# Kernel optimization log

Measured on AMD Instinct MI355X. Metric: run time of the kernel, lower is better.

The kernel has to match this reference:

```python
import jax, jax.numpy as jnp
import numpy as np
from jax import lax

GAMMA = 2.0
BLANK = 0
NEG = -1e30  # log-space 'zero'
T, B, C, L = 1000, 64, 256, 100


def setup_inputs() -> dict:
    key = jax.random.key(0)
    k1, k2 = jax.random.split(key)
    # valid log-probabilities, as produced by a model's log_softmax head
    log_probs = jax.nn.log_softmax(jax.random.normal(k1, (T, B, C), dtype=jnp.float32), axis=-1)
    # concatenated targets, blank (0) excluded as CTC requires
    targets = jax.random.randint(k2, (B * L,), 1, C, dtype=jnp.int32)
    input_lengths = jnp.full((B,), T, dtype=jnp.int32)
    target_lengths = jnp.full((B,), L, dtype=jnp.int32)
    return {"log_probs": log_probs, "targets": targets,
            "input_lengths": input_lengths, "target_lengths": target_lengths}


def _ctc_loss(log_probs, targets2d, input_lengths, target_lengths):
    # log_probs: (T,B,C); targets2d: (B,L). Returns per-sample NLL (B,).
    Tt, Bb, _ = log_probs.shape
    Ll = targets2d.shape[1]
    S = 2 * Ll + 1  # extended label sequence: blank interleaved
    ext = jnp.full((Bb, S), BLANK, dtype=jnp.int32).at[:, 1::2].set(targets2d)
    # emission log-probs for each extended symbol: (T,B,S)
    emit = jnp.take_along_axis(log_probs, jnp.broadcast_to(ext[None], (Tt, Bb, S)), axis=2)
    # skip-transition allowed where symbol is non-blank and differs from s-2
    allow2 = jnp.concatenate(
        [jnp.zeros((Bb, 2), bool), (ext[:, 2:] != BLANK) & (ext[:, 2:] != ext[:, :-2])], axis=1)

    def shiftk(a, k):
        return jnp.pad(a, ((0, 0), (k, 0)), constant_values=NEG)[:, :S]

    alpha0 = jnp.full((Bb, S), NEG, jnp.float32).at[:, 0].set(emit[0, :, 0]).at[:, 1].set(emit[0, :, 1])

    def step(alpha, e):
        a1 = shiftk(alpha, 1)
        a2 = jnp.where(allow2, shiftk(alpha, 2), NEG)
        m = jnp.maximum(jnp.maximum(alpha, a1), a2)
        new = m + jnp.log(jnp.exp(alpha - m) + jnp.exp(a1 - m) + jnp.exp(a2 - m)) + e
        return new, new

    _, rest = lax.scan(step, alpha0, emit[1:])
    alphas = jnp.concatenate([alpha0[None], rest], axis=0)  # (T,B,S)
    b = jnp.arange(Bb)
    last = alphas[input_lengths - 1, b]  # (B,S) at each sample's final step
    ll = jnp.logaddexp(last[b, 2 * target_lengths], last[b, 2 * target_lengths - 1])
    # zero_infinity=True semantics
    return jnp.where(ll > NEG / 2, -ll, 0.0)


def reference(log_probs, targets, input_lengths, target_lengths):
    targets2d = targets.reshape(B, L)
    loss = _ctc_loss(log_probs, targets2d, input_lengths, target_lengths)  # (B,)
    # focal weights: mean-over-time prob of each target symbol (computed under no_grad in torch)
    mean_probs = jnp.exp(log_probs).mean(axis=0)  # (B,C)
    target_probs = lax.stop_gradient(
        jnp.take_along_axis(mean_probs, targets2d, axis=1).reshape(-1))  # (B*L,)
    focal_weight = (1.0 - target_probs) ** GAMMA
    # torch broadcasting quirk: (total,) * (B,1) -> (B,total); mean over all
    return (focal_weight[None, :] * loss[:, None]).mean()
```

## Files before the change

kernel.cpp:

```cpp
#include <hip/hip_runtime.h>
#include <cstdint>

#define T_DIM 1000
#define B_DIM 64
#define C_DIM 256
#define L_DIM 100
#define S_DIM (2 * L_DIM + 1)
#define CH 32
#define NPROD 7
#define RPW 5
#define MEAN_BLOCKS 192

typedef float f32x4 __attribute__((ext_vector_type(4)));

#define DPP_I(x, ctrl) __builtin_amdgcn_update_dpp(0, (x), (ctrl), 0xF, 0xF, true)
#define DPP_F(x, ctrl) __int_as_float(DPP_I(__float_as_int(x), (ctrl)))


#define DSR(dst, addr, OFF) \
    asm volatile("ds_read_b32 %0, %1 offset:" OFF : "=v"(dst) : "v"(addr))
#define ISS(s, OFF) do { DSR(pb##s, apb, OFF); DSR(qa##s, aq1, OFF); DSR(qb##s, aq3, OFF); } while (0)
#define W(N) do { asm volatile("s_waitcnt lgkmcnt(" N ")"); __builtin_amdgcn_sched_barrier(0); } while (0)
#define STP(s) step(pb##s, qa##s, qb##s)

__device__ __forceinline__ float wave_max_dpp(float x) {
    x = fmaxf(x, DPP_F(x, 0x111));
    x = fmaxf(x, DPP_F(x, 0x112));
    x = fmaxf(x, DPP_F(x, 0x114));
    x = fmaxf(x, DPP_F(x, 0x118));
    x = fmaxf(x, DPP_F(x, 0x142));
    x = fmaxf(x, DPP_F(x, 0x143));
    return __int_as_float(__builtin_amdgcn_readlane(__float_as_int(x), 63));
}

__global__ __launch_bounds__(512, 1) void ctc_fused(
        const float* __restrict__ lp,
        const int* __restrict__ tgt,
        const int* __restrict__ il,
        const int* __restrict__ tl,
        float* __restrict__ ws_mean,
        float* __restrict__ ws_loss) {
    const int blk = blockIdx.x;
    const uint32_t rstride = B_DIM * C_DIM;

    if (blk >= B_DIM) {
        const int mb = blk - B_DIM;
        const int b = mb / 3;
        const int slice = mb % 3;
        const int half = threadIdx.x >> 8;
        const int c = threadIdx.x & 255;
        const int h0 = (slice < 2) ? 170 : 165;
        const int scount = (slice < 2) ? 335 : 330;
        const int start = slice * 335 + (half ? h0 : 0);
        const int cnt = half ? (scount - h0) : h0;
        const float* p = lp + (size_t)b * C_DIM + c + (size_t)start * rstride;
        float s0 = 0.f, s1 = 0.f, s2 = 0.f, s3 = 0.f, s4 = 0.f;
        for (int t = 0; t < cnt; t += 5) {
            s0 += __expf(p[(size_t)(t + 0) * rstride]);
            s1 += __expf(p[(size_t)(t + 1) * rstride]);
            s2 += __expf(p[(size_t)(t + 2) * rstride]);
            s3 += __expf(p[(size_t)(t + 3) * rstride]);
            s4 += __expf(p[(size_t)(t + 4) * rstride]);
        }
        atomicAdd(&ws_mean[b * C_DIM + c], (s0 + s1 + s2 + s3 + s4) * (1.0f / T_DIM));
        return;
    }

    __shared__ __align__(16) float rows[2][CH][C_DIM];

    const int tid = threadIdx.x;
    const int lane = tid & 63;
    const int wave = tid >> 6;
    const int b = blk;
    const int* trow = tgt + b * L_DIM;
    const int ilen = il[b];
    const int tlen = tl[b];

    const int i1 = 2 * lane;
    const int i3 = 2 * lane + 1;
    const int c1 = (i1 < L_DIM) ? trow[i1] : 0;
    const int c3 = (i3 < L_DIM) ? trow[i3] : 0;
    const int c1m = (i1 >= 1 && i1 - 1 < L_DIM) ? trow[i1 - 1] : -1;
    const float m1 = ((i1 >= 1) && (c1 != c1m)) ? 1.0f : 0.0f;
    const float m3 = (c3 != c1) ? 1.0f : 0.0f;

    const float f0 = (4 * lane + 0 < S_DIM) ? 1.0f : 0.0f;
    const float f1 = (4 * lane + 1 < S_DIM) ? 1.0f : 0.0f;
    const float f2 = (4 * lane + 2 < S_DIM) ? 1.0f : 0.0f;
    const float f3 = (4 * lane + 3 < S_DIM) ? 1.0f : 0.0f;

    const float* base = lp + (size_t)b * C_DIM;

    float a0 = 0.f, a1 = 0.f, a2 = 0.f, a3 = 0.f;
    {
        float i0 = __expf(base[0]);
        float i1v = __expf(base[c1]);
        if (lane == 0 && wave == 0) { a0 = i0; a1 = i1v; }
    }
    float ls = 0.f;

    auto produce = [&](int cc) {
        const int p = cc & 1;
        const int tstart = 1 + cc * CH;
        f32x4 v[RPW];
#pragma unroll
        for (int k = 0; k < RPW; ++k) {
            const int d = (wave - 1) + NPROD * k;
            if (d < CH) {
                int t = tstart + d; t = (t < ilen) ? t : (ilen - 1);
                v[k] = *(const f32x4*)(base + (size_t)t * rstride + (lane << 2));
            } else {
                v[k] = (f32x4){0.f, 0.f, 0.f, 0.f};
            }
        }
        asm volatile("" : "+v"(v[0]), "+v"(v[1]), "+v"(v[2]), "+v"(v[3]), "+v"(v[4]));
#pragma unroll
        for (int k = 0; k < RPW; ++k) {
            const int d = (wave - 1) + NPROD * k;
            if (d < CH) {
                f32x4 e;
                e.x = __expf(v[k].x); e.y = __expf(v[k].y);
                e.z = __expf(v[k].z); e.w = __expf(v[k].w);
                *(f32x4*)&rows[p][d][lane << 2] = e;
            }
        }
    };

    auto step = [&](float pb, float p1e, float p3e) {
        const float p3 = DPP_F(a3, 0x138);
        const float a01 = a0 + a1;
        const float n0 = (a0 + p3) * pb;
        const float n1 = fmaf(m1, p3, a01) * p1e;
        const float n2 = (a2 + a1) * pb;
        const float n3 = (fmaf(m3, a1, a2) + a3) * p3e;
        a0 = n0; a1 = n1; a2 = n2; a3 = n3;
    };

#define RENORM() do {                                                       \
        a0 *= f0; a1 *= f1; a2 *= f2; a3 *= f3;                             \
        const float mx = wave_max_dpp(fmaxf(fmaxf(a0, a1), fmaxf(a2, a3))); \
        const float inv = __builtin_amdgcn_rcpf(mx);                        \
        ls -= __logf(inv);                                                  \
        a0 *= inv; a1 *= inv; a2 *= inv; a3 *= inv;                         \
    } while (0)

    auto consume = [&](int cc) {
        const int p = cc & 1;
        const int tstart = 1 + cc * CH;
        if (tstart + CH <= ilen) {
            const uint32_t lbase =
                (uint32_t)(uintptr_t)(&rows[0][0][0]) + (uint32_t)(p * (CH * C_DIM * 4));
            uint32_t apb = lbase;
            uint32_t aq1 = lbase + ((uint32_t)c1 << 2);
            uint32_t aq3 = lbase + ((uint32_t)c3 << 2);
            float pb0, pb1, pb2, pb3, pb4;
            float qa0, qa1, qa2, qa3, qa4;
            float qb0, qb1, qb2, qb3, qb4;
            ISS(0, "0"); ISS(1, "1024"); ISS(2, "2048"); ISS(3, "3072"); ISS(4, "4096");
            W("12"); STP(0); ISS(0, "5120");
            W("12"); STP(1); ISS(1, "6144");
            W("12"); STP(2); ISS(2, "7168");
            W("12"); STP(3); ISS(3, "8192");
            W("12"); STP(4); ISS(4, "9216");
            W("12"); STP(0); ISS(0, "10240");
            W("12"); STP(1); ISS(1, "11264");
            W("12"); STP(2); ISS(2, "12288"); RENORM();
            W("12"); STP(3); ISS(3, "13312");
            W("12"); STP(4); ISS(4, "14336");
            W("12"); STP(0); ISS(0, "15360");
            W("12"); STP(1); ISS(1, "16384");
            W("12"); STP(2); ISS(2, "17408");
            W("12"); STP(3); ISS(3, "18432");
            W("12"); STP(4); ISS(4, "19456");
            W("12"); STP(0); ISS(0, "20480"); RENORM();
            W("12"); STP(1); ISS(1, "21504");
            W("12"); STP(2); ISS(2, "22528");
            W("12"); STP(3); ISS(3, "23552");
            W("12"); STP(4); ISS(4, "24576");
            W("12"); STP(0); ISS(0, "25600");
            W("12"); STP(1); ISS(1, "26624");
            W("12"); STP(2); ISS(2, "27648");
            W("12"); STP(3); ISS(3, "28672"); RENORM();
            W("12"); STP(4); ISS(4, "29696");
            W("12"); STP(0); ISS(0, "30720");
            W("12"); STP(1); ISS(1, "31744");
            W("12"); STP(2);
            W("9");  STP(3);
            W("6");  STP(4);
            W("3");  STP(0);
            W("0");  STP(1); RENORM();
        } else {
#pragma unroll
            for (int d = 0; d < CH; ++d) {
                if (tstart + d < ilen) {
                    step(rows[p][d][0], rows[p][d][c1], rows[p][d][c3]);
                    if ((d & 7) == 7) RENORM();
                }
            }
        }
    };

    const int nchunks = (ilen - 1 + CH - 1) / CH;
    if (wave != 0) produce(0);
    __syncthreads();
    if (wave == 0) __builtin_amdgcn_s_setprio(1);
    for (int c = 0; c < nchunks; ++c) {
        if (wave != 0) produce(c + 1);
        else consume(c);
        __syncthreads();
    }
    if (wave == 0) __builtin_amdgcn_s_setprio(0);
#undef RENORM

    if (wave != 0) return;

    const int s_hi = 2 * tlen;
    const int s_lo = 2 * tlen - 1;
    const int slot_hi = s_hi & 3, lane_hi = min(s_hi >> 2, 63);
    const int slot_lo = s_lo & 3, lane_lo = min(s_lo >> 2, 63);
    float ch = (slot_hi == 0) ? a0 : (slot_hi == 1) ? a1 : (slot_hi == 2) ? a2 : a3;
    float cl = (slot_lo == 0) ? a0 : (slot_lo == 1) ? a1 : (slot_lo == 2) ? a2 : a3;
    const float vh = __shfl(ch, lane_hi, 64);
    const float vl = __shfl(cl, lane_lo, 64);
    if (lane == 0) {
        const float s = vh + vl;
        const float loss = (s > 0.f) ? -(__logf(s) + ls) : 0.0f;
        ws_loss[b] = loss;
    }
}

__global__ __launch_bounds__(256) void ctc_finalize(
        const float* __restrict__ ws_mean, const float* __restrict__ ws_loss,
        const int* __restrict__ tgt, float* __restrict__ out) {
    const int tid = threadIdx.x;
    float fsum = 0.f;
#pragma unroll
    for (int k = 0; k < (B_DIM * L_DIM) / 256; ++k) {
        const int j = tid + k * 256;
        const int b = j / L_DIM;
        const int c = tgt[j];
        const float p = ws_mean[b * C_DIM + c];
        const float w = 1.0f - p;
        fsum += w * w;
    }
    float lsum = (tid < B_DIM) ? ws_loss[tid] : 0.f;
#pragma unroll
    for (int off = 32; off > 0; off >>= 1) {
        fsum += __shfl_down(fsum, off, 64);
        lsum += __shfl_down(lsum, off, 64);
    }
    __shared__ float sf[4], sl[4];
    const int w = tid >> 6;
    if ((tid & 63) == 0) { sf[w] = fsum; sl[w] = lsum; }
    __syncthreads();
    if (tid == 0) {
        const float F = sf[0] + sf[1] + sf[2] + sf[3];
        const float Lo = sl[0] + sl[1] + sl[2] + sl[3];
        out[0] = (F / (float)(B_DIM * L_DIM)) * (Lo / (float)B_DIM);
    }
}

extern "C" void kernel_launch(void* const* d_in, const int* in_sizes, int n_in,
                              void* d_out, int out_size, void* d_ws, size_t ws_size,
                              hipStream_t stream) {
    const float* lp = (const float*)d_in[0];
    const int* tgt = (const int*)d_in[1];
    const int* il = (const int*)d_in[2];
    const int* tl = (const int*)d_in[3];
    float* ws_mean = (float*)d_ws;
    float* ws_loss = ws_mean + B_DIM * C_DIM;

    hipMemsetAsync(ws_mean, 0, B_DIM * C_DIM * sizeof(float), stream);
    ctc_fused<<<dim3(B_DIM + MEAN_BLOCKS), dim3(512), 0, stream>>>(
        lp, tgt, il, tl, ws_mean, ws_loss);
    ctc_finalize<<<dim3(1), dim3(256), 0, stream>>>(ws_mean, ws_loss, tgt, (float*)d_out);
}
```

Before: 138.4 us.

## Split mean-probability pass into separate vectorized kernel ahead of CTC recursion

The per-(batch,class) mean-exp reduction moves out of the extra blocks of the fused CTC kernel into its own kernel launched first. It uses 512 blocks of 256 threads, float4 loads and an LDS reduction across four waves. The CTC kernel now launches only the 64 recursion blocks. This serializes the memory-bound mean pass before the latency-bound CTC recursion instead of overlapping them, and trades that lost overlap for a faster, better-coalesced mean pass.

Measured after the change: 149.1 us. 1.08x slower.

```diff
diff --git a/kernel.cpp b/kernel.cpp
--- a/kernel.cpp
+++ b/kernel.cpp
@@ -9,13 +9,11 @@
 #define CH 32
 #define NPROD 7
 #define RPW 5
-#define MEAN_BLOCKS 192
 
 typedef float f32x4 __attribute__((ext_vector_type(4)));
 
 #define DPP_I(x, ctrl) __builtin_amdgcn_update_dpp(0, (x), (ctrl), 0xF, 0xF, true)
 #define DPP_F(x, ctrl) __int_as_float(DPP_I(__float_as_int(x), (ctrl)))
-
 
 #define DSR(dst, addr, OFF) \
     asm volatile("ds_read_b32 %0, %1 offset:" OFF : "=v"(dst) : "v"(addr))
@@ -33,38 +31,37 @@
     return __int_as_float(__builtin_amdgcn_readlane(__float_as_int(x), 63));
 }
 
+__global__ __launch_bounds__(256) void mean_pass(
+        const float* __restrict__ lp, float* __restrict__ ws_mean) {
+    const int mb = blockIdx.x;
+    const int b = mb >> 3;
+    const int t0 = (mb & 7) * 125;
+    const int lane = threadIdx.x & 63;
+    const int wv = threadIdx.x >> 6;
+    const uint32_t rstride = B_DIM * C_DIM;
+    const float* p = lp + (size_t)b * C_DIM + (lane << 2);
+    f32x4 s = {0.f, 0.f, 0.f, 0.f};
+    for (int t = t0 + wv; t < t0 + 125; t += 4) {
+        f32x4 v = *(const f32x4*)(p + (size_t)t * rstride);
+        s.x += __expf(v.x); s.y += __expf(v.y);
+        s.z += __expf(v.z); s.w += __expf(v.w);
+    }
+    __shared__ float sums[4][C_DIM];
+    *(f32x4*)&sums[wv][lane << 2] = s;
+    __syncthreads();
+    const int c = threadIdx.x;
+    const float tot = sums[0][c] + sums[1][c] + sums[2][c] + sums[3][c];
+    atomicAdd(&ws_mean[b * C_DIM + c], tot * (1.0f / T_DIM));
+}
+
 __global__ __launch_bounds__(512, 1) void ctc_fused(
         const float* __restrict__ lp,
         const int* __restrict__ tgt,
         const int* __restrict__ il,
         const int* __restrict__ tl,
-        float* __restrict__ ws_mean,
         float* __restrict__ ws_loss) {
     const int blk = blockIdx.x;
     const uint32_t rstride = B_DIM * C_DIM;
-
-    if (blk >= B_DIM) {
-        const int mb = blk - B_DIM;
-        const int b = mb / 3;
-        const int slice = mb % 3;
-        const int half = threadIdx.x >> 8;
-        const int c = threadIdx.x & 255;
-        const int h0 = (slice < 2) ? 170 : 165;
-        const int scount = (slice < 2) ? 335 : 330;
-        const int start = slice * 335 + (half ? h0 : 0);
-        const int cnt = half ? (scount - h0) : h0;
-        const float* p = lp + (size_t)b * C_DIM + c + (size_t)start * rstride;
-        float s0 = 0.f, s1 = 0.f, s2 = 0.f, s3 = 0.f, s4 = 0.f;
-        for (int t = 0; t < cnt; t += 5) {
-            s0 += __expf(p[(size_t)(t + 0) * rstride]);
-            s1 += __expf(p[(size_t)(t + 1) * rstride]);
-            s2 += __expf(p[(size_t)(t + 2) * rstride]);
-            s3 += __expf(p[(size_t)(t + 3) * rstride]);
-            s4 += __expf(p[(size_t)(t + 4) * rstride]);
-        }
-        atomicAdd(&ws_mean[b * C_DIM + c], (s0 + s1 + s2 + s3 + s4) * (1.0f / T_DIM));
-        return;
-    }
 
     __shared__ __align__(16) float rows[2][CH][C_DIM];
 
@@ -271,7 +268,7 @@
     float* ws_loss = ws_mean + B_DIM * C_DIM;
 
     hipMemsetAsync(ws_mean, 0, B_DIM * C_DIM * sizeof(float), stream);
-    ctc_fused<<<dim3(B_DIM + MEAN_BLOCKS), dim3(512), 0, stream>>>(
-        lp, tgt, il, tl, ws_mean, ws_loss);
+    mean_pass<<<dim3(B_DIM * 8), dim3(256), 0, stream>>>(lp, ws_mean);
+    ctc_fused<<<dim3(B_DIM), dim3(512), 0, stream>>>(lp, tgt, il, tl, ws_loss);
     ctc_finalize<<<dim3(1), dim3(256), 0, stream>>>(ws_mean, ws_loss, tgt, (float*)d_out);
 }
```
